# Kernel optimization log

Hardware: AMD Instinct MI355X
Metric: run time of the kernel (lower is better)

## Reference

```python
import jax, jax.numpy as jnp
import numpy as np

B, ORG, L = 128, 4, 2048
C1, C2 = 128, 64
K0, K1, K2 = 7, 5, 3
VQD, VQN = 64, 1024
CARD, NG = 32, 8
EPS = 1e-5


def _conv(x, w, groups=1):
    # 1D conv, stride 1, 'same' padding (k-1)//2, NCH layout, weight (O, I/g, K)
    p = (w.shape[-1] - 1) // 2
    return jax.lax.conv_general_dilated(
        x, w, (1,), [(p, p)],
        dimension_numbers=('NCH', 'OIH', 'NCH'), feature_group_count=groups)


def _tconv(x, w):
    # ConvTranspose1d(stride=1, padding=(k-1)//2) == conv with channel-transposed, spatially flipped kernel
    return _conv(x, jnp.flip(jnp.transpose(w, (1, 0, 2)), -1))


def _gn(x, g, b, groups=NG):
    Bx, C, T = x.shape
    xr = x.reshape(Bx, groups, C // groups, T)
    mu = xr.mean((2, 3), keepdims=True)
    var = xr.var((2, 3), keepdims=True)
    xn = ((xr - mu) * jax.lax.rsqrt(var + EPS)).reshape(Bx, C, T)
    return xn * g[None, :, None] + b[None, :, None]


def setup_inputs() -> dict:
    key = jax.random.key(0)
    ks = iter(jax.random.split(key, 32))
    w = lambda *s: jax.random.normal(next(ks), s, jnp.float32) * 0.05
    ones = lambda n: jnp.ones((n,), jnp.float32)
    zeros = lambda n: jnp.zeros((n,), jnp.float32)
    D = C1 // 2  # ResNeXt bottleneck width
    return dict(
        x=jax.random.normal(next(ks), (B, ORG, L), jnp.float32),
        w0=w(C1, ORG, K0), g0_g=ones(C1), g0_b=zeros(C1),
        wxa=w(D, C1, 1), gxa_g=ones(D), gxa_b=zeros(D),
        wxb=w(D, D // CARD, K1), gxb_g=ones(D), gxb_b=zeros(D),
        wxc=w(C1, D, 1), gxc_g=ones(C1), gxc_b=zeros(C1),
        w2=w(C2, C1, K2), bn2_g=ones(C2), bn2_b=zeros(C2),
        embed_w=jax.random.uniform(next(ks), (VQN, VQD), jnp.float32, -1.0 / VQD, 1.0 / VQD),
        wd2=w(C2, C1, K2), gd2_g=ones(C1), gd2_b=zeros(C1),
        wd1a=w(C1, C1, K1), gd1a_g=ones(C1), gd1a_b=zeros(C1),
        wd1b=w(C1, C1, K1), gd1b_g=ones(C1), gd1b_b=zeros(C1),
        wd0=w(C1, ORG, K0), bd0=zeros(ORG),
    )


def reference(x, w0, g0_g, g0_b, wxa, gxa_g, gxa_b, wxb, gxb_g, gxb_b,
              wxc, gxc_g, gxc_b, w2, bn2_g, bn2_b, embed_w,
              wd2, gd2_g, gd2_b, wd1a, gd1a_g, gd1a_b, wd1b, gd1b_g, gd1b_b,
              wd0, bd0):
    selu = jax.nn.selu

    # ---- encoder ----
    h = selu(_gn(_conv(x, w0), g0_g, g0_b))  # res0

    def resx(h):  # ResNeXt bottleneck, shared weights (module reuses self.resx)
        y = selu(_gn(_conv(h, wxa), gxa_g, gxa_b))
        y = selu(_gn(_conv(y, wxb, groups=CARD), gxb_g, gxb_b))
        y = _gn(_conv(y, wxc), gxc_g, gxc_b)
        return selu(h + y)

    pool = lambda t: t.reshape(t.shape[0], t.shape[1], -1, 2).max(-1)  # MaxPool1d(2)
    h = pool(resx(h))
    h = pool(resx(h))
    # res2: conv + BatchNorm (eval mode, running stats 0/1 -> affine)
    h = _conv(h, w2) * bn2_g[None, :, None] + bn2_b[None, :, None]

    # ---- vector quantization (vqc=True: quantize channel vectors) ----
    Bh, C, T = h.shape  # C == VQD
    Z = jnp.transpose(h, (0, 2, 1)).reshape(-1, VQD)  # [N, vq_dim]
    d = (jnp.sum(Z * Z, 1, keepdims=True) - 2.0 * (Z @ embed_w.T)
         + jnp.sum(embed_w * embed_w, 1)[None, :])  # [N, vq_num] squared L2
    j = jnp.argmin(d, axis=1)
    W_j = embed_w[j]
    commit_loss = jnp.mean(jnp.sum((Z - jax.lax.stop_gradient(W_j)) ** 2, -1))
    vq_loss = jnp.mean(jnp.sum((jax.lax.stop_gradient(Z) - W_j) ** 2, -1))
    hq = jnp.transpose(W_j.reshape(Bh, T, C), (0, 2, 1))  # back to [B, C, T]

    # ---- decoder ----
    up = lambda t: jnp.repeat(t, 2, axis=-1)  # nearest Upsample(x2)

    def deres1(h):  # basic residual block, shared weights (module reuses self.deres1)
        y = selu(_gn(_tconv(h, wd1a), gd1a_g, gd1a_b))
        y = _gn(_tconv(y, wd1b), gd1b_g, gd1b_b)
        return selu(h + y)

    h = selu(_gn(_tconv(hq, wd2), gd2_g, gd2_b))  # deres2
    h = deres1(up(h))
    h = deres1(up(h))
    recon = _tconv(h, wd0) + bd0[None, :, None]  # deres0 (with bias)
    return recon, commit_loss, vq_loss
```

## Files before the change

kernel.cpp:

```cpp
#include <hip/hip_runtime.h>
#include <math.h>

static constexpr int B_   = 128;
static constexpr int ORG_ = 4;
static constexpr int L_   = 2048;
static constexpr int C1_  = 128;
static constexpr int C2_  = 64;
static constexpr int NG_  = 8;
static constexpr int VQD_ = 64;
static constexpr int VQN_ = 1024;
static constexpr long PTS_ = (long)B_ * (L_ / 4);

typedef __attribute__((ext_vector_type(8))) short bf16x8;
typedef __attribute__((ext_vector_type(4))) float f32x4;

__device__ __forceinline__ float selu_f(float x) {
    const float scale = 1.0507009873554805f;
    const float alpha = 1.6732632423543772f;
    return scale * (x > 0.f ? x : alpha * expm1f(x));
}
__device__ __forceinline__ unsigned short f2bf(float x) {
    unsigned u = __float_as_uint(x);
    u = (u + 0x7FFFu + ((u >> 16) & 1u)) >> 16;
    return (unsigned short)u;
}

__global__ void wprep_kernel(const float* __restrict__ w, float* __restrict__ wT,
                             int CO, int cig, int K, int so, int si, int sk, int koff)
{
    int idx = blockIdx.x * 256 + threadIdx.x;
    int total = cig * K * CO;
    if (idx >= total) return;
    int o = idx % CO;
    int r = idx / CO;
    int i = r / K, k = r % K;
    wT[idx] = w[(long)o * so + (long)i * si + (long)k * sk + koff];
}

__global__ void wprep_mfma_kernel(const float* __restrict__ w, unsigned short* __restrict__ wb)
{
    int idx = blockIdx.x * 256 + threadIdx.x;
    if (idx >= 5 * 16 * 128 * 8) return;
    int j  = idx & 7;
    int o  = (idx >> 3) & 127;
    int kk = idx >> 10;
    int ig = kk & 3, ic = (kk >> 2) & 3, k = kk >> 4;
    int i  = ic * 32 + ig * 8 + j;
    wb[idx] = f2bf(w[(long)i * (128 * 5) + o * 5 + (4 - k)]);
}

__global__ void fill_kernel(float* p, float v, int n)
{
    int i = blockIdx.x * 256 + threadIdx.x;
    if (i < n) p[i] = v;
}

template<int K, int CO, int NTHR, int TT, int OT, int VQ>
__global__ __launch_bounds__(NTHR) void conv_tile_kernel(
    const float* __restrict__ in, const float* __restrict__ wT,
    const float* __restrict__ scale, const float* __restrict__ bias,
    float* __restrict__ out,
    int CI, int T, int cig, int cog,
    const float* __restrict__ ist, const float* __restrict__ ig,
    const float* __restrict__ ibt, int icpg, int iselu,
    const float* __restrict__ res,
    float* __restrict__ vbest, int* __restrict__ vbj, int jbase)
{
    constexpr int P    = (K - 1) / 2;
    constexpr int SPAN = TT + K - 1;
    constexpr int RS   = (SPAN + 3) & ~3;
    constexpr int NO   = CO / OT;
    constexpr int NT   = (CO * TT) / (NTHR * OT);
    constexpr int XW   = NT + K - 1;
    extern __shared__ float lds[];

    const int tile = blockIdx.x;
    const int b    = blockIdx.y;
    const int t0g  = tile * TT;
    const float* inb = in + (long)b * CI * T;

    for (int idx = threadIdx.x; idx < CI * SPAN; idx += NTHR) {
        int c = idx / SPAN, j = idx % SPAN;
        int tt = t0g + j - P;
        float v = 0.f;
        if (tt >= 0 && tt < T) {
            v = inb[(long)c * T + tt];
            if (ist) {
                const float* s = &ist[2 * (b * NG_ + c / icpg)];
                v = (v - s[0]) * s[1] * ig[c] + ibt[c];
                if (res) v += res[((long)b * CI + c) * T + tt];
                if (iselu) v = selu_f(v);
            }
        }
        lds[c * RS + j] = v;
    }
    __syncthreads();

    const int o0   = (threadIdx.x % NO) * OT;
    const int slot = threadIdx.x / NO;
    const int t0   = slot * NT;
    const int g    = o0 / cog;
    const float* wrow = wT + o0;

    float acc[OT][NT];
#pragma unroll
    for (int oo = 0; oo < OT; ++oo)
#pragma unroll
        for (int u = 0; u < NT; ++u) acc[oo][u] = 0.f;

    for (int i = 0; i < cig; ++i) {
        const int irow = g * cig + i;
        float xin[(XW + 3) & ~3];
        if constexpr (NT % 4 == 0) {
            constexpr int X4 = (XW + 3) / 4;
            const float4* l4 = reinterpret_cast<const float4*>(&lds[irow * RS + t0]);
#pragma unroll
            for (int j = 0; j < X4; ++j) {
                float4 v = l4[j];
                xin[4 * j]     = v.x;
                xin[4 * j + 1] = v.y;
                xin[4 * j + 2] = v.z;
                xin[4 * j + 3] = v.w;
            }
        } else {
#pragma unroll
            for (int j = 0; j < XW; ++j) xin[j] = lds[irow * RS + t0 + j];
        }
        float wk[OT][K];
#pragma unroll
        for (int oo = 0; oo < OT; ++oo)
#pragma unroll
            for (int k = 0; k < K; ++k) wk[oo][k] = wrow[(i * K + k) * CO + oo];
#pragma unroll
        for (int oo = 0; oo < OT; ++oo)
#pragma unroll
            for (int u = 0; u < NT; ++u)
#pragma unroll
                for (int k = 0; k < K; ++k)
                    acc[oo][u] = fmaf(xin[u + k], wk[oo][k], acc[oo][u]);
    }

    if constexpr (VQ) {
        const int lane = threadIdx.x & 63;
#pragma unroll
        for (int u = 0; u < NT; ++u) {
            float bv = 3.4e38f;
            int bj = 0;
#pragma unroll
            for (int oo = 0; oo < OT; ++oo) {
                const int o = o0 + oo;
                float sv = fmaf(acc[oo][u], scale[o], bias[o]);
                if (sv < bv) { bv = sv; bj = jbase + o; }
            }
#pragma unroll
            for (int off = 1; off < 64; off <<= 1) {
                float v2 = __shfl_xor(bv, off);
                int   j2 = __shfl_xor(bj, off);
                if (v2 < bv || (v2 == bv && j2 < bj)) { bv = v2; bj = j2; }
            }
            if (lane == 0) {
                long n = (long)b * T + t0g + t0 + u;
                vbest[n] = bv;
                vbj[n]   = bj;
            }
        }
    } else {
#pragma unroll
        for (int oo = 0; oo < OT; ++oo) {
            const int o = o0 + oo;
            const float sc = scale ? scale[o] : 1.f;
            const float bi = bias  ? bias[o]  : 0.f;
            float* ob = out + ((long)b * CO + o) * T + t0g + t0;
#pragma unroll
            for (int u = 0; u < NT; ++u) ob[u] = acc[oo][u] * sc + bi;
        }
    }
}

__global__ __launch_bounds__(256) void conv_epi7_kernel(
    const float* __restrict__ in, const float* __restrict__ wT,
    const float* __restrict__ bias, float* __restrict__ out, int T,
    const float* __restrict__ ist, const float* __restrict__ ig_,
    const float* __restrict__ ibt, int icpg,
    const float* __restrict__ res)
{
    __shared__ float wlds[128 * 7 * 4];
    __shared__ float rows[4][80];

    for (int idx = threadIdx.x; idx < 128 * 7 * 4; idx += 256)
        wlds[idx] = wT[idx];
    __syncthreads();

    const int wid  = threadIdx.x >> 6;
    const int lane = threadIdx.x & 63;
    const int b    = blockIdx.y;
    const int t0w  = blockIdx.x * 256 + wid * 64;
    const int t    = t0w + lane;
    float* row = rows[wid];
    const long base = (long)b * 128 * T;

    float acc0 = 0.f, acc1 = 0.f, acc2 = 0.f, acc3 = 0.f;

    for (int ci = 0; ci < 128; ++ci) {
        const float* s = &ist[2 * (b * NG_ + ci / icpg)];
        const float mu = s[0], rs = s[1];
        const float gc = ig_[ci], bc = ibt[ci];
        const long cbase = base + (long)ci * T;

        float v = in[cbase + t];
        v = (v - mu) * rs * gc + bc;
        v += res[cbase + t];
        v = selu_f(v);
        row[3 + lane] = v;

        if (lane < 3 || lane >= 61) {
            int th   = (lane < 3) ? (t0w - 3 + lane) : (t0w + 3 + lane);
            int ridx = (lane < 3) ? lane : (lane + 6);
            float h = 0.f;
            if (th >= 0 && th < T) {
                h = in[cbase + th];
                h = (h - mu) * rs * gc + bc;
                h += res[cbase + th];
                h = selu_f(h);
            }
            row[ridx] = h;
        }

        float xin[7];
#pragma unroll
        for (int j = 0; j < 7; ++j) xin[j] = row[lane + j];
#pragma unroll
        for (int k = 0; k < 7; ++k) {
            float4 w4 = *(const float4*)&wlds[(ci * 7 + k) * 4];
            acc0 = fmaf(xin[k], w4.x, acc0);
            acc1 = fmaf(xin[k], w4.y, acc1);
            acc2 = fmaf(xin[k], w4.z, acc2);
            acc3 = fmaf(xin[k], w4.w, acc3);
        }
    }

    out[((long)b * 4 + 0) * T + t] = acc0 * 1.f + bias[0];
    out[((long)b * 4 + 1) * T + t] = acc1 * 1.f + bias[1];
    out[((long)b * 4 + 2) * T + t] = acc2 * 1.f + bias[2];
    out[((long)b * 4 + 3) * T + t] = acc3 * 1.f + bias[3];
}

__global__ __launch_bounds__(256) void conv_mfma5_kernel(
    const float* __restrict__ in, const unsigned short* __restrict__ wb,
    float* __restrict__ out, int T,
    const float* __restrict__ ist, const float* __restrict__ ig_,
    const float* __restrict__ ibt, int icpg)
{
    constexpr int SPAN = 68, RSI = 136;
    __shared__ unsigned short xlds[SPAN * RSI];

    const int t0g = blockIdx.x * 64;
    const int b   = blockIdx.y;
    const float* inb = in + (long)b * 128 * T;

    for (int idx = threadIdx.x; idx < 128 * SPAN; idx += 256) {
        int i = idx / SPAN, j = idx % SPAN;
        int tt = t0g + j - 2;
        float v = 0.f;
        if (tt >= 0 && tt < T) {
            v = inb[(long)i * T + tt];
            if (ist) {
                const float* s = &ist[2 * (b * NG_ + i / icpg)];
                v = selu_f((v - s[0]) * s[1] * ig_[i] + ibt[i]);
            }
        }
        xlds[j * RSI + i] = f2bf(v);
    }
    __syncthreads();

    const int lane = threadIdx.x & 63;
    const int wid  = threadIdx.x >> 6;
    const int tw   = wid * 16;
    const int mr   = lane & 15;
    const int kg   = lane >> 4;

    f32x4 acc[8];
#pragma unroll
    for (int ot = 0; ot < 8; ++ot) acc[ot] = (f32x4){0.f, 0.f, 0.f, 0.f};

#pragma unroll
    for (int k = 0; k < 5; ++k) {
#pragma unroll
        for (int ic = 0; ic < 4; ++ic) {
            bf16x8 a = *(const bf16x8*)&xlds[(tw + mr + k) * RSI + ic * 32 + kg * 8];
            const unsigned short* wp = wb + (((k * 16 + ic * 4 + kg) * 128) + mr) * 8;
#pragma unroll
            for (int ot = 0; ot < 8; ++ot) {
                bf16x8 bfr = *(const bf16x8*)(wp + ot * 16 * 8);
                acc[ot] = __builtin_amdgcn_mfma_f32_16x16x32_bf16(a, bfr, acc[ot], 0, 0, 0);
            }
        }
    }

#pragma unroll
    for (int ot = 0; ot < 8; ++ot) {
        int o = ot * 16 + mr;
        float4 v = make_float4(acc[ot][0], acc[ot][1], acc[ot][2], acc[ot][3]);
        *(float4*)&out[((long)b * 128 + o) * T + t0g + tw + kg * 4] = v;
    }
}

__global__ __launch_bounds__(256) void gn_stats_kernel(
    const float* __restrict__ x, float* __restrict__ stats,
    int C, int T, int G)
{
    const int bg = blockIdx.x;
    const int cpg = C / G;
    const int b = bg / G, g = bg % G;
    const float* base = x + ((long)b * C + (long)g * cpg) * T;
    const long n4 = (long)cpg * T / 4;
    const float4* b4 = (const float4*)base;
    float s = 0.f, ss = 0.f;
    for (long i = threadIdx.x; i < n4; i += blockDim.x) {
        float4 v = b4[i];
        s += v.x + v.y + v.z + v.w;
        ss += v.x * v.x + v.y * v.y + v.z * v.z + v.w * v.w;
    }
#pragma unroll
    for (int off = 32; off; off >>= 1) {
        s  += __shfl_down(s, off);
        ss += __shfl_down(ss, off);
    }
    __shared__ float sh_s[4], sh_ss[4];
    const int wid = threadIdx.x >> 6, lane = threadIdx.x & 63;
    if (lane == 0) { sh_s[wid] = s; sh_ss[wid] = ss; }
    __syncthreads();
    if (threadIdx.x == 0) {
        float S = 0.f, SS = 0.f;
        for (int i = 0; i < 4; ++i) { S += sh_s[i]; SS += sh_ss[i]; }
        float inv_n = 1.f / (float)((long)cpg * T);
        float mu  = S * inv_n;
        float var = SS * inv_n - mu * mu;
        stats[2 * bg]     = mu;
        stats[2 * bg + 1] = rsqrtf(var + 1e-5f);
    }
}

__global__ __launch_bounds__(256) void pool_fused_kernel(
    const float* __restrict__ x, const float* __restrict__ xst,
    const float* __restrict__ xg, const float* __restrict__ xb, int xcpg,
    const float* __restrict__ r, const float* __restrict__ rst,
    const float* __restrict__ rg, const float* __restrict__ rb, int rcpg, int rselu,
    float* __restrict__ out, int C, int Tout, long total)
{
    for (long idx = blockIdx.x * (long)blockDim.x + threadIdx.x; idx < total;
         idx += (long)gridDim.x * blockDim.x) {
        const int to = (int)(idx % Tout);
        const int c  = (int)((idx / Tout) % C);
        const int b  = (int)(idx / ((long)Tout * C));
        const long base = ((long)b * C + c) * (2 * Tout);
        const float* sx = &xst[2 * (b * NG_ + c / xcpg)];
        const float xgc = sx[1] * xg[c], xbc = xb[c] - sx[0] * sx[1] * xg[c];
        float rgc = 1.f, rbc = 0.f;
        if (rst) {
            const float* sr = &rst[2 * (b * NG_ + c / rcpg)];
            rgc = sr[1] * rg[c]; rbc = rb[c] - sr[0] * sr[1] * rg[c];
        }
        float f[2];
#pragma unroll
        for (int q = 0; q < 2; ++q) {
            long t = base + 2 * to + q;
            float rv = r[t] * rgc + rbc;
            if (rst && rselu) rv = selu_f(rv);
            f[q] = selu_f(x[t] * xgc + xbc + rv);
        }
        out[((long)b * C + c) * Tout + to] = fmaxf(f[0], f[1]);
    }
}

__global__ __launch_bounds__(256) void up_fused_kernel(
    const float* __restrict__ x, const float* __restrict__ xst,
    const float* __restrict__ xg, const float* __restrict__ xb, int xcpg,
    const float* __restrict__ res,
    float* __restrict__ out, int C, int Tin, long total)
{
    for (long idx = blockIdx.x * (long)blockDim.x + threadIdx.x; idx < total;
         idx += (long)gridDim.x * blockDim.x) {
        const int t = (int)(idx % Tin);
        const int c = (int)((idx / Tin) % C);
        const int b = (int)(idx / ((long)Tin * C));
        const float* s = &xst[2 * (b * NG_ + c / xcpg)];
        float v = (x[idx] - s[0]) * s[1] * xg[c] + xb[c];
        if (res) v += res[idx];
        v = selu_f(v);
        float2* o2 = (float2*)(out + (((long)b * C + c) * Tin + t) * 2);
        *o2 = make_float2(v, v);
    }
}

__global__ void wnorm_kernel(const float* __restrict__ codes, float* __restrict__ wn)
{
    int j = blockIdx.x * 256 + threadIdx.x;
    if (j >= VQN_) return;
    const float* c = codes + (long)j * VQD_;
    float s = 0.f;
#pragma unroll
    for (int i = 0; i < VQD_; ++i) s = fmaf(c[i], c[i], s);
    wn[j] = s;
}

__global__ void vq_combine_kernel(const float* __restrict__ vb, const int* __restrict__ vj,
                                  int* __restrict__ bjs, long stride, int NP)
{
    int n = blockIdx.x * 256 + threadIdx.x;
    if (n >= NP) return;
    float best = vb[n];
    int bj = vj[n];
#pragma unroll
    for (int s = 1; s < 4; ++s) {
        float v = vb[(long)s * stride + n];
        if (v < best) { best = v; bj = vj[(long)s * stride + n]; }
    }
    bjs[n] = bj;
}

__global__ __launch_bounds__(256) void vq_gather_kernel(
    const float* __restrict__ h, const float* __restrict__ codes,
    const int* __restrict__ bjs, float* __restrict__ hq, float* __restrict__ loss,
    int T)
{
    const int n0 = blockIdx.x * 64;
    const int b  = n0 / T;
    const int tb = n0 % T;
    __shared__ int sbj[64];
    if (threadIdx.x < 64) sbj[threadIdx.x] = bjs[n0 + threadIdx.x];
    __syncthreads();

    float l = 0.f;
#pragma unroll
    for (int r = 0; r < (VQD_ * 64) / 256; ++r) {
        int idx = r * 256 + (int)threadIdx.x;
        int c  = idx >> 6, tl = idx & 63;
        float wv = codes[(long)sbj[tl] * VQD_ + c];
        long off = ((long)b * VQD_ + c) * T + tb + tl;
        hq[off] = wv;
        float df = h[off] - wv;
        l = fmaf(df, df, l);
    }
#pragma unroll
    for (int off = 32; off; off >>= 1) l += __shfl_down(l, off);
    if ((threadIdx.x & 63) == 0) atomicAdd(loss, l);
}

__global__ void zero_kernel(float* p) { p[0] = 0.f; }

__global__ void finalize_kernel(const float* __restrict__ loss, float* __restrict__ out,
                                float invNP, long off)
{
    float v = loss[0] * invNP;
    out[off]     = v;
    out[off + 1] = v;
}

static inline int nblk(long total, int thr = 256, long cap = 262144) {
    long b = (total + thr - 1) / thr;
    if (b > cap) b = cap;
    if (b < 1) b = 1;
    return (int)b;
}
static inline int ldsz(int CI, int K, int TT = 64) {
    int span = TT + K - 1;
    int rs = (span + 3) & ~3;
    return CI * rs * 4;
}

struct WT {
    long w0, wxa, wxb, wxc, w2, wd2, wd0, total;
};
static WT wt_offsets() {
    WT o; long p = 0;
    o.w0   = p; p += (long)ORG_ * 7 * C1_;
    o.wxa  = p; p += (long)C1_ * 1 * (C1_ / 2);
    o.wxb  = p; p += 2L * 5 * (C1_ / 2);
    o.wxc  = p; p += (long)(C1_ / 2) * 1 * C1_;
    o.w2   = p; p += (long)C1_ * 3 * C2_;
    o.wd2  = p; p += (long)C2_ * 3 * C1_;
    o.wd0  = p; p += (long)C1_ * 7 * ORG_;
    o.total = p;
    return o;
}

static void run_chunk(const float* x, const float* const* W, const float* wt,
                      const WT& wo, const unsigned short* wbA, const unsigned short* wbB,
                      const float* wn, const float* wts, const float* neg2,
                      float* vbest4, int* vbj4, int* bjs, float* out,
                      float* A, float* Bb, float* Cc, float* st, float* lossbuf,
                      int Bc, long nbuf, hipStream_t stream)
{
    const float* g0_g  = W[1];
    const float* g0_b  = W[2];
    const float* gxa_g = W[4];
    const float* gxa_b = W[5];
    const float* gxb_g = W[7];
    const float* gxb_b = W[8];
    const float* gxc_g = W[10];
    const float* gxc_b = W[11];
    const float* bn2_g = W[13];
    const float* bn2_b = W[14];
    const float* embed = W[15];
    const float* gd2_g = W[17];
    const float* gd2_b = W[18];
    const float* gd1a_g= W[20];
    const float* gd1a_b= W[21];
    const float* gd1b_g= W[23];
    const float* gd1b_b= W[24];
    const float* bd0   = W[26];

    const int D_ = C1_ / 2;
    const int SLOT = 2048;
    float* st0 = st + 0 * SLOT;
    float* st1 = st + 1 * SLOT;
    float* st2 = st + 2 * SLOT;
    float* st3 = st + 3 * SLOT;
    float* st4 = st + 4 * SLOT;
    float* st5 = st + 5 * SLOT;
    float* st6 = st + 6 * SLOT;

    const int nbg = Bc * NG_;

    int T = L_;

    conv_tile_kernel<7, 128, 512, 64, 1, 0><<<dim3(T / 64, Bc), 512, ldsz(ORG_, 7), stream>>>(
        x, wt + wo.w0, nullptr, nullptr, A, ORG_, T, ORG_, C1_,
        nullptr, nullptr, nullptr, 0, 0, nullptr, nullptr, nullptr, 0);
    gn_stats_kernel<<<nbg, 256, 0, stream>>>(A, st0, C1_, T, NG_);

    conv_tile_kernel<1, 64, 512, 64, 2, 0><<<dim3(T / 64, Bc), 512, ldsz(C1_, 1), stream>>>(
        A, wt + wo.wxa, nullptr, nullptr, Bb, C1_, T, C1_, D_,
        st0, g0_g, g0_b, C1_ / NG_, 1, nullptr, nullptr, nullptr, 0);
    gn_stats_kernel<<<nbg, 256, 0, stream>>>(Bb, st1, D_, T, NG_);

    conv_tile_kernel<5, 64, 512, 64, 1, 0><<<dim3(T / 64, Bc), 512, ldsz(D_, 5), stream>>>(
        Bb, wt + wo.wxb, nullptr, nullptr, Bb + nbuf / 2, D_, T, 2, 2,
        st1, gxa_g, gxa_b, D_ / NG_, 1, nullptr, nullptr, nullptr, 0);
    gn_stats_kernel<<<nbg, 256, 0, stream>>>(Bb + nbuf / 2, st2, D_, T, NG_);

    conv_tile_kernel<1, 128, 512, 64, 2, 0><<<dim3(T / 64, Bc), 512, ldsz(D_, 1), stream>>>(
        Bb + nbuf / 2, wt + wo.wxc, nullptr, nullptr, Cc, D_, T, D_, C1_,
        st2, gxb_g, gxb_b, D_ / NG_, 1, nullptr, nullptr, nullptr, 0);
    gn_stats_kernel<<<nbg, 256, 0, stream>>>(Cc, st3, C1_, T, NG_);

    {
        int Tout = T / 2;
        long tt = (long)Bc * C1_ * Tout;
        pool_fused_kernel<<<nblk(tt), 256, 0, stream>>>(
            Cc, st3, gxc_g, gxc_b, C1_ / NG_,
            A, st0, g0_g, g0_b, C1_ / NG_, 1,
            Bb, C1_, Tout, tt);
        T = Tout;
    }

    conv_tile_kernel<1, 64, 512, 64, 2, 0><<<dim3(T / 64, Bc), 512, ldsz(C1_, 1), stream>>>(
        Bb, wt + wo.wxa, nullptr, nullptr, Cc, C1_, T, C1_, D_,
        nullptr, nullptr, nullptr, 0, 0, nullptr, nullptr, nullptr, 0);
    gn_stats_kernel<<<nbg, 256, 0, stream>>>(Cc, st1, D_, T, NG_);

    conv_tile_kernel<5, 64, 512, 64, 1, 0><<<dim3(T / 64, Bc), 512, ldsz(D_, 5), stream>>>(
        Cc, wt + wo.wxb, nullptr, nullptr, Cc + nbuf / 2, D_, T, 2, 2,
        st1, gxa_g, gxa_b, D_ / NG_, 1, nullptr, nullptr, nullptr, 0);
    gn_stats_kernel<<<nbg, 256, 0, stream>>>(Cc + nbuf / 2, st2, D_, T, NG_);

    conv_tile_kernel<1, 128, 512, 64, 2, 0><<<dim3(T / 64, Bc), 512, ldsz(D_, 1), stream>>>(
        Cc + nbuf / 2, wt + wo.wxc, nullptr, nullptr, A, D_, T, D_, C1_,
        st2, gxb_g, gxb_b, D_ / NG_, 1, nullptr, nullptr, nullptr, 0);
    gn_stats_kernel<<<nbg, 256, 0, stream>>>(A, st3, C1_, T, NG_);

    {
        int Tout = T / 2;
        long tt = (long)Bc * C1_ * Tout;
        pool_fused_kernel<<<nblk(tt), 256, 0, stream>>>(
            A, st3, gxc_g, gxc_b, C1_ / NG_,
            Bb, nullptr, nullptr, nullptr, 0, 0,
            Cc, C1_, Tout, tt);
        T = Tout;
    }

    conv_tile_kernel<3, 64, 512, 64, 1, 0><<<dim3(T / 64, Bc), 512, ldsz(C1_, 3), stream>>>(
        Cc, wt + wo.w2, bn2_g, bn2_b, Bb, C1_, T, C1_, C2_,
        nullptr, nullptr, nullptr, 0, 0, nullptr, nullptr, nullptr, 0);

    {
        int NP = Bc * T;
        for (int s = 0; s < 4; ++s) {
            conv_tile_kernel<1, 256, 512, 64, 4, 1><<<dim3(T / 64, Bc), 512,
                                                      ldsz(VQD_, 1), stream>>>(
                Bb, wts + (long)s * 256 * VQD_, neg2, wn + s * 256, nullptr,
                VQD_, T, VQD_, 256,
                nullptr, nullptr, nullptr, 0, 0, nullptr,
                vbest4 + (long)s * PTS_, vbj4 + (long)s * PTS_, s * 256);
        }
        vq_combine_kernel<<<(NP + 255) / 256, 256, 0, stream>>>(vbest4, vbj4, bjs, PTS_, NP);
        vq_gather_kernel<<<NP / 64, 256, 0, stream>>>(Bb, embed, bjs, A, lossbuf, T);
    }

    conv_tile_kernel<3, 128, 512, 64, 1, 0><<<dim3(T / 64, Bc), 512, ldsz(C2_, 3), stream>>>(
        A, wt + wo.wd2, nullptr, nullptr, Bb, C2_, T, C2_, C1_,
        nullptr, nullptr, nullptr, 0, 0, nullptr, nullptr, nullptr, 0);
    gn_stats_kernel<<<nbg, 256, 0, stream>>>(Bb, st4, C1_, T, NG_);

    {
        long tt = (long)Bc * C1_ * T;
        up_fused_kernel<<<nblk(tt), 256, 0, stream>>>(
            Bb, st4, gd2_g, gd2_b, C1_ / NG_, nullptr, Cc, C1_, T, tt);
        T *= 2;
    }

    conv_mfma5_kernel<<<dim3(T / 64, Bc), 256, 0, stream>>>(
        Cc, wbA, A, T, nullptr, nullptr, nullptr, 0);
    gn_stats_kernel<<<nbg, 256, 0, stream>>>(A, st5, C1_, T, NG_);

    conv_mfma5_kernel<<<dim3(T / 64, Bc), 256, 0, stream>>>(
        A, wbB, Bb, T, st5, gd1a_g, gd1a_b, C1_ / NG_);
    gn_stats_kernel<<<nbg, 256, 0, stream>>>(Bb, st6, C1_, T, NG_);

    {
        long tt = (long)Bc * C1_ * T;
        up_fused_kernel<<<nblk(tt), 256, 0, stream>>>(
            Bb, st6, gd1b_g, gd1b_b, C1_ / NG_, Cc, A, C1_, T, tt);
        T *= 2;
    }

    conv_mfma5_kernel<<<dim3(T / 64, Bc), 256, 0, stream>>>(
        A, wbA, Cc, T, nullptr, nullptr, nullptr, 0);
    gn_stats_kernel<<<nbg, 256, 0, stream>>>(Cc, st5, C1_, T, NG_);

    conv_mfma5_kernel<<<dim3(T / 64, Bc), 256, 0, stream>>>(
        Cc, wbB, Bb, T, st5, gd1a_g, gd1a_b, C1_ / NG_);
    gn_stats_kernel<<<nbg, 256, 0, stream>>>(Bb, st6, C1_, T, NG_);

    conv_epi7_kernel<<<dim3(T / 256, Bc), 256, 0, stream>>>(
        Bb, wt + wo.wd0, bd0, out, T,
        st6, gd1b_g, gd1b_b, C1_ / NG_, A);
}

extern "C" void kernel_launch(void* const* d_in, const int* in_sizes, int n_in,
                              void* d_out, int out_size, void* d_ws, size_t ws_size,
                              hipStream_t stream) {
    const float* x = (const float*)d_in[0];
    const float* W[27];
    for (int i = 0; i < 27; ++i) W[i] = (const float*)d_in[i + 1];

    float* out = (float*)d_out;
    const WT wo = wt_offsets();

    const long WT_F32  = 262144;
    const long WB_F32  = 2 * 81920 / 2;
    const long WTS_F32 = VQN_ * VQD_;
    const long ST_F32  = 8 * 2048;
    const long VQ_F32  = 4 * PTS_ + 4 * PTS_ + PTS_;
    const long FIXED = WT_F32 + WB_F32 + 1024 + WTS_F32 + 256 + ST_F32 + 64 + VQ_F32;
    int Bc = 0;
    for (int cand = B_; cand >= 1; cand >>= 1) {
        size_t need = ((size_t)FIXED + (size_t)3 * cand * C1_ * L_) * sizeof(float);
        if (need <= ws_size) { Bc = cand; break; }
    }
    if (Bc == 0) return;

    float* wt            = (float*)d_ws;
    unsigned short* wbA  = (unsigned short*)(wt + WT_F32);
    unsigned short* wbB  = wbA + 81920;
    float* wn            = wt + WT_F32 + WB_F32;
    float* wts           = wn + 1024;
    float* neg2          = wts + WTS_F32;
    float* st            = neg2 + 256;
    float* lossbuf       = st + ST_F32;
    float* vbest4        = lossbuf + 64;
    int*   vbj4          = (int*)(vbest4 + 4 * PTS_);
    int*   bjs           = vbj4 + 4 * PTS_;
    const long nbuf = (long)Bc * C1_ * L_;
    float* A  = (float*)(bjs + PTS_);
    float* Bb = A + nbuf;
    float* Cc = Bb + nbuf;

    const int D_ = C1_ / 2;

    auto prep = [&](const float* w, long off, int CO, int cig, int K,
                    int so, int si, int sk, int koff) {
        int total = cig * K * CO;
        wprep_kernel<<<(total + 255) / 256, 256, 0, stream>>>(
            w, wt + off, CO, cig, K, so, si, sk, koff);
    };
    prep(W[0],  wo.w0,   C1_, ORG_, 7, ORG_ * 7, 7,        1,  0);
    prep(W[3],  wo.wxa,  D_,  C1_,  1, C1_,      1,        1,  0);
    prep(W[6],  wo.wxb,  D_,  2,    5, 2 * 5,    5,        1,  0);
    prep(W[9],  wo.wxc,  C1_, D_,   1, D_,       1,        1,  0);
    prep(W[12], wo.w2,   C2_, C1_,  3, C1_ * 3,  3,        1,  0);
    prep(W[16], wo.wd2,  C1_, C2_,  3, 3,        C1_ * 3, -1,  2);
    prep(W[25], wo.wd0,  ORG_, C1_, 7, 7,        ORG_ * 7, -1, 6);
    wprep_mfma_kernel<<<81920 / 256, 256, 0, stream>>>(W[19], wbA);
    wprep_mfma_kernel<<<81920 / 256, 256, 0, stream>>>(W[22], wbB);
    wnorm_kernel<<<(VQN_ + 255) / 256, 256, 0, stream>>>(W[15], wn);
    for (int q = 0; q < 4; ++q) {
        wprep_kernel<<<(256 * VQD_ + 255) / 256, 256, 0, stream>>>(
            W[15] + (long)q * 256 * VQD_, wts + (long)q * 256 * VQD_,
            256, VQD_, 1, VQD_, 1, 1, 0);
    }
    fill_kernel<<<1, 256, 0, stream>>>(neg2, -2.f, 256);

    zero_kernel<<<1, 1, 0, stream>>>(lossbuf);

    for (int b0 = 0; b0 < B_; b0 += Bc) {
        const float* xc = x + (long)b0 * ORG_ * L_;
        float* outc = out + (long)b0 * ORG_ * L_;
        run_chunk(xc, W, wt, wo, wbA, wbB, wn, wts, neg2, vbest4, vbj4, bjs,
                  outc, A, Bb, Cc, st, lossbuf, Bc, nbuf, stream);
    }

    {
        float invNP = 1.f / (float)(B_ * (L_ / 4));
        finalize_kernel<<<1, 1, 0, stream>>>(lossbuf, out, invNP, (long)out_size - 2);
    }
}
```

Before: 2.229 ms.

## Store decoder activations in bf16 to halve memory traffic across decoder stages

Decoder intermediate buffers (upsample outputs, MFMA conv outputs, residuals) are now stored as bf16 instead of fp32. The conv, GroupNorm-stats, upsample and final 7-tap conv kernels change to read and write bf16, and a new vectorized bf16 GroupNorm stats kernel is added. This roughly halves the bytes moved by the memory-bound decoder passes, at the cost of extra rounding in activations and residuals. Separately, the VQ distance kernel processes more output channels per thread with a narrower shuffle reduction.

```diff
diff --git a/kernel.cpp b/kernel.cpp
--- a/kernel.cpp
+++ b/kernel.cpp
@@ -23,6 +23,9 @@
     unsigned u = __float_as_uint(x);
     u = (u + 0x7FFFu + ((u >> 16) & 1u)) >> 16;
     return (unsigned short)u;
+}
+__device__ __forceinline__ float bf2f(unsigned short u) {
+    return __uint_as_float((unsigned)u << 16);
 }
 
 __global__ void wprep_kernel(const float* __restrict__ w, float* __restrict__ wT,
@@ -141,6 +144,7 @@
     }
 
     if constexpr (VQ) {
+        constexpr int RW = (NO >= 64) ? 64 : 32;
         const int lane = threadIdx.x & 63;
 #pragma unroll
         for (int u = 0; u < NT; ++u) {
@@ -153,12 +157,12 @@
                 if (sv < bv) { bv = sv; bj = jbase + o; }
             }
 #pragma unroll
-            for (int off = 1; off < 64; off <<= 1) {
+            for (int off = 1; off < RW; off <<= 1) {
                 float v2 = __shfl_xor(bv, off);
                 int   j2 = __shfl_xor(bj, off);
                 if (v2 < bv || (v2 == bv && j2 < bj)) { bv = v2; bj = j2; }
             }
-            if (lane == 0) {
+            if ((lane & (RW - 1)) == 0) {
                 long n = (long)b * T + t0g + t0 + u;
                 vbest[n] = bv;
                 vbj[n]   = bj;
@@ -178,11 +182,11 @@
 }
 
 __global__ __launch_bounds__(256) void conv_epi7_kernel(
-    const float* __restrict__ in, const float* __restrict__ wT,
+    const unsigned short* __restrict__ in, const float* __restrict__ wT,
     const float* __restrict__ bias, float* __restrict__ out, int T,
     const float* __restrict__ ist, const float* __restrict__ ig_,
     const float* __restrict__ ibt, int icpg,
-    const float* __restrict__ res)
+    const unsigned short* __restrict__ res)
 {
     __shared__ float wlds[128 * 7 * 4];
     __shared__ float rows[4][80];
@@ -207,9 +211,9 @@
         const float gc = ig_[ci], bc = ibt[ci];
         const long cbase = base + (long)ci * T;
 
-        float v = in[cbase + t];
+        float v = bf2f(in[cbase + t]);
         v = (v - mu) * rs * gc + bc;
-        v += res[cbase + t];
+        v += bf2f(res[cbase + t]);
         v = selu_f(v);
         row[3 + lane] = v;
 
@@ -218,9 +222,9 @@
             int ridx = (lane < 3) ? lane : (lane + 6);
             float h = 0.f;
             if (th >= 0 && th < T) {
-                h = in[cbase + th];
+                h = bf2f(in[cbase + th]);
                 h = (h - mu) * rs * gc + bc;
-                h += res[cbase + th];
+                h += bf2f(res[cbase + th]);
                 h = selu_f(h);
             }
             row[ridx] = h;
@@ -239,15 +243,15 @@
         }
     }
 
-    out[((long)b * 4 + 0) * T + t] = acc0 * 1.f + bias[0];
-    out[((long)b * 4 + 1) * T + t] = acc1 * 1.f + bias[1];
-    out[((long)b * 4 + 2) * T + t] = acc2 * 1.f + bias[2];
-    out[((long)b * 4 + 3) * T + t] = acc3 * 1.f + bias[3];
+    out[((long)b * 4 + 0) * T + t] = acc0 + bias[0];
+    out[((long)b * 4 + 1) * T + t] = acc1 + bias[1];
+    out[((long)b * 4 + 2) * T + t] = acc2 + bias[2];
+    out[((long)b * 4 + 3) * T + t] = acc3 + bias[3];
 }
 
 __global__ __launch_bounds__(256) void conv_mfma5_kernel(
-    const float* __restrict__ in, const unsigned short* __restrict__ wb,
-    float* __restrict__ out, int T,
+    const unsigned short* __restrict__ in, const unsigned short* __restrict__ wb,
+    unsigned short* __restrict__ out, int T,
     const float* __restrict__ ist, const float* __restrict__ ig_,
     const float* __restrict__ ibt, int icpg)
 {
@@ -256,20 +260,21 @@
 
     const int t0g = blockIdx.x * 64;
     const int b   = blockIdx.y;
-    const float* inb = in + (long)b * 128 * T;
+    const unsigned short* inb = in + (long)b * 128 * T;
 
     for (int idx = threadIdx.x; idx < 128 * SPAN; idx += 256) {
         int i = idx / SPAN, j = idx % SPAN;
         int tt = t0g + j - 2;
-        float v = 0.f;
+        unsigned short raw = 0;
         if (tt >= 0 && tt < T) {
-            v = inb[(long)i * T + tt];
+            raw = inb[(long)i * T + tt];
             if (ist) {
                 const float* s = &ist[2 * (b * NG_ + i / icpg)];
-                v = selu_f((v - s[0]) * s[1] * ig_[i] + ibt[i]);
+                float v = selu_f((bf2f(raw) - s[0]) * s[1] * ig_[i] + ibt[i]);
+                raw = f2bf(v);
             }
         }
-        xlds[j * RSI + i] = f2bf(v);
+        xlds[j * RSI + i] = raw;
     }
     __syncthreads();
 
@@ -300,8 +305,12 @@
 #pragma unroll
     for (int ot = 0; ot < 8; ++ot) {
         int o = ot * 16 + mr;
-        float4 v = make_float4(acc[ot][0], acc[ot][1], acc[ot][2], acc[ot][3]);
-        *(float4*)&out[((long)b * 128 + o) * T + t0g + tw + kg * 4] = v;
+        ushort4 v;
+        v.x = f2bf(acc[ot][0]);
+        v.y = f2bf(acc[ot][1]);
+        v.z = f2bf(acc[ot][2]);
+        v.w = f2bf(acc[ot][3]);
+        *(ushort4*)&out[((long)b * 128 + o) * T + t0g + tw + kg * 4] = v;
     }
 }
 
@@ -341,6 +350,48 @@
     }
 }
 
+__global__ __launch_bounds__(256) void gn_stats_bf16_kernel(
+    const unsigned short* __restrict__ x, float* __restrict__ stats,
+    int C, int T, int G)
+{
+    const int bg = blockIdx.x;
+    const int cpg = C / G;
+    const int b = bg / G, g = bg % G;
+    const unsigned short* base = x + ((long)b * C + (long)g * cpg) * T;
+    const long n8 = (long)cpg * T / 8;
+    const uint4* b8 = (const uint4*)base;
+    float s = 0.f, ss = 0.f;
+    for (long i = threadIdx.x; i < n8; i += blockDim.x) {
+        uint4 v = b8[i];
+        unsigned ws[4] = {v.x, v.y, v.z, v.w};
+#pragma unroll
+        for (int q = 0; q < 4; ++q) {
+            float f0 = __uint_as_float(ws[q] << 16);
+            float f1 = __uint_as_float(ws[q] & 0xFFFF0000u);
+            s += f0 + f1;
+            ss += f0 * f0 + f1 * f1;
+        }
+    }
+#pragma unroll
+    for (int off = 32; off; off >>= 1) {
+        s  += __shfl_down(s, off);
+        ss += __shfl_down(ss, off);
+    }
+    __shared__ float sh_s[4], sh_ss[4];
+    const int wid = threadIdx.x >> 6, lane = threadIdx.x & 63;
+    if (lane == 0) { sh_s[wid] = s; sh_ss[wid] = ss; }
+    __syncthreads();
+    if (threadIdx.x == 0) {
+        float S = 0.f, SS = 0.f;
+        for (int i = 0; i < 4; ++i) { S += sh_s[i]; SS += sh_ss[i]; }
+        float inv_n = 1.f / (float)((long)cpg * T);
+        float mu  = S * inv_n;
+        float var = SS * inv_n - mu * mu;
+        stats[2 * bg]     = mu;
+        stats[2 * bg + 1] = rsqrtf(var + 1e-5f);
+    }
+}
+
 __global__ __launch_bounds__(256) void pool_fused_kernel(
     const float* __restrict__ x, const float* __restrict__ xst,
     const float* __restrict__ xg, const float* __restrict__ xb, int xcpg,
@@ -373,11 +424,12 @@
     }
 }
 
+template<int INBF>
 __global__ __launch_bounds__(256) void up_fused_kernel(
-    const float* __restrict__ x, const float* __restrict__ xst,
+    const void* __restrict__ x_, const float* __restrict__ xst,
     const float* __restrict__ xg, const float* __restrict__ xb, int xcpg,
-    const float* __restrict__ res,
-    float* __restrict__ out, int C, int Tin, long total)
+    const unsigned short* __restrict__ res,
+    unsigned short* __restrict__ out, int C, int Tin, long total)
 {
     for (long idx = blockIdx.x * (long)blockDim.x + threadIdx.x; idx < total;
          idx += (long)gridDim.x * blockDim.x) {
@@ -385,11 +437,14 @@
         const int c = (int)((idx / Tin) % C);
         const int b = (int)(idx / ((long)Tin * C));
         const float* s = &xst[2 * (b * NG_ + c / xcpg)];
-        float v = (x[idx] - s[0]) * s[1] * xg[c] + xb[c];
-        if (res) v += res[idx];
+        float v = INBF ? bf2f(((const unsigned short*)x_)[idx])
+                       : ((const float*)x_)[idx];
+        v = (v - s[0]) * s[1] * xg[c] + xb[c];
+        if (res) v += bf2f(res[idx]);
         v = selu_f(v);
-        float2* o2 = (float2*)(out + (((long)b * C + c) * Tin + t) * 2);
-        *o2 = make_float2(v, v);
+        unsigned short h = f2bf(v);
+        unsigned pack = (unsigned)h | ((unsigned)h << 16);
+        *(unsigned*)(out + (((long)b * C + c) * Tin + t) * 2) = pack;
     }
 }
 
@@ -521,7 +576,12 @@
     float* st5 = st + 5 * SLOT;
     float* st6 = st + 6 * SLOT;
 
+    unsigned short* Au  = (unsigned short*)A;
+    unsigned short* Bbu = (unsigned short*)Bb;
+    unsigned short* Ccu = (unsigned short*)Cc;
+
     const int nbg = Bc * NG_;
+    const int cpg1 = C1_ / NG_;
 
     int T = L_;
 
@@ -532,7 +592,7 @@
 
     conv_tile_kernel<1, 64, 512, 64, 2, 0><<<dim3(T / 64, Bc), 512, ldsz(C1_, 1), stream>>>(
         A, wt + wo.wxa, nullptr, nullptr, Bb, C1_, T, C1_, D_,
-        st0, g0_g, g0_b, C1_ / NG_, 1, nullptr, nullptr, nullptr, 0);
+        st0, g0_g, g0_b, cpg1, 1, nullptr, nullptr, nullptr, 0);
     gn_stats_kernel<<<nbg, 256, 0, stream>>>(Bb, st1, D_, T, NG_);
 
     conv_tile_kernel<5, 64, 512, 64, 1, 0><<<dim3(T / 64, Bc), 512, ldsz(D_, 5), stream>>>(
@@ -549,8 +609,8 @@
         int Tout = T / 2;
         long tt = (long)Bc * C1_ * Tout;
         pool_fused_kernel<<<nblk(tt), 256, 0, stream>>>(
-            Cc, st3, gxc_g, gxc_b, C1_ / NG_,
-            A, st0, g0_g, g0_b, C1_ / NG_, 1,
+            Cc, st3, gxc_g, gxc_b, cpg1,
+            A, st0, g0_g, g0_b, cpg1, 1,
             Bb, C1_, Tout, tt);
         T = Tout;
     }
@@ -574,7 +634,7 @@
         int Tout = T / 2;
         long tt = (long)Bc * C1_ * Tout;
         pool_fused_kernel<<<nblk(tt), 256, 0, stream>>>(
-            A, st3, gxc_g, gxc_b, C1_ / NG_,
+            A, st3, gxc_g, gxc_b, cpg1,
             Bb, nullptr, nullptr, nullptr, 0, 0,
             Cc, C1_, Tout, tt);
         T = Tout;
@@ -587,7 +647,7 @@
     {
         int NP = Bc * T;
         for (int s = 0; s < 4; ++s) {
-            conv_tile_kernel<1, 256, 512, 64, 4, 1><<<dim3(T / 64, Bc), 512,
+            conv_tile_kernel<1, 256, 512, 64, 8, 1><<<dim3(T / 64, Bc), 512,
                                                       ldsz(VQD_, 1), stream>>>(
                 Bb, wts + (long)s * 256 * VQD_, neg2, wn + s * 256, nullptr,
                 VQD_, T, VQD_, 256,
@@ -605,37 +665,37 @@
 
     {
         long tt = (long)Bc * C1_ * T;
-        up_fused_kernel<<<nblk(tt), 256, 0, stream>>>(
-            Bb, st4, gd2_g, gd2_b, C1_ / NG_, nullptr, Cc, C1_, T, tt);
+        up_fused_kernel<0><<<nblk(tt), 256, 0, stream>>>(
+            Bb, st4, gd2_g, gd2_b, cpg1, nullptr, Ccu, C1_, T, tt);
         T *= 2;
     }
 
     conv_mfma5_kernel<<<dim3(T / 64, Bc), 256, 0, stream>>>(
-        Cc, wbA, A, T, nullptr, nullptr, nullptr, 0);
-    gn_stats_kernel<<<nbg, 256, 0, stream>>>(A, st5, C1_, T, NG_);
+        Ccu, wbA, Au, T, nullptr, nullptr, nullptr, 0);
+    gn_stats_bf16_kernel<<<nbg, 256, 0, stream>>>(Au, st5, C1_, T, NG_);
 
     conv_mfma5_kernel<<<dim3(T / 64, Bc), 256, 0, stream>>>(
-        A, wbB, Bb, T, st5, gd1a_g, gd1a_b, C1_ / NG_);
-    gn_stats_kernel<<<nbg, 256, 0, stream>>>(Bb, st6, C1_, T, NG_);
+        Au, wbB, Bbu, T, st5, gd1a_g, gd1a_b, cpg1);
+    gn_stats_bf16_kernel<<<nbg, 256, 0, stream>>>(Bbu, st6, C1_, T, NG_);
 
     {
         long tt = (long)Bc * C1_ * T;
-        up_fused_kernel<<<nblk(tt), 256, 0, stream>>>(
-            Bb, st6, gd1b_g, gd1b_b, C1_ / NG_, Cc, A, C1_, T, tt);
+        up_fused_kernel<1><<<nblk(tt), 256, 0, stream>>>(
+            Bbu, st6, gd1b_g, gd1b_b, cpg1, Ccu, Au, C1_, T, tt);
         T *= 2;
     }
 
     conv_mfma5_kernel<<<dim3(T / 64, Bc), 256, 0, stream>>>(
-        A, wbA, Cc, T, nullptr, nullptr, nullptr, 0);
-    gn_stats_kernel<<<nbg, 256, 0, stream>>>(Cc, st5, C1_, T, NG_);
+        Au, wbA, Ccu, T, nullptr, nullptr, nullptr, 0);
+    gn_stats_bf16_kernel<<<nbg, 256, 0, stream>>>(Ccu, st5, C1_, T, NG_);
 
     conv_mfma5_kernel<<<dim3(T / 64, Bc), 256, 0, stream>>>(
-        Cc, wbB, Bb, T, st5, gd1a_g, gd1a_b, C1_ / NG_);
-    gn_stats_kernel<<<nbg, 256, 0, stream>>>(Bb, st6, C1_, T, NG_);
+        Ccu, wbB, Bbu, T, st5, gd1a_g, gd1a_b, cpg1);
+    gn_stats_bf16_kernel<<<nbg, 256, 0, stream>>>(Bbu, st6, C1_, T, NG_);
 
     conv_epi7_kernel<<<dim3(T / 256, Bc), 256, 0, stream>>>(
-        Bb, wt + wo.wd0, bd0, out, T,
-        st6, gd1b_g, gd1b_b, C1_ / NG_, A);
+        Bbu, wt + wo.wd0, bd0, out, T,
+        st6, gd1b_g, gd1b_b, cpg1, Au);
 }
 
 extern "C" void kernel_launch(void* const* d_in, const int* in_sizes, int n_in,
```

New measurement: 2.283 ms. +2.4%, slower.
